# Kernel optimization log

Hardware: AMD Instinct MI355X
Metric: run time of the kernel (lower is better)

Reference implementation:

```python
import jax, jax.numpy as jnp
import numpy as np

B, C, H, W = 8, 16, 64, 64
O = 32
K = 3
STRIDE = 1
HO = (H - K) // STRIDE + 1  # 62
WO = (W - K) // STRIDE + 1  # 62
BIAS_VAL = 0.1


def setup_inputs() -> dict:
    key = jax.random.key(0)
    k1, k2 = jax.random.split(key)
    x = jax.random.normal(k1, (B, C, H, W), dtype=jnp.float32)
    # per-location weights: (1, O, C, Ho, Wo, K*K) in torch; drop leading 1
    weight = jax.random.normal(k2, (O, C, HO, WO, K * K), dtype=jnp.float32)
    bias = jnp.full((1, O, HO, WO), BIAS_VAL, dtype=jnp.float32)
    return {"x": x, "weight": weight, "bias": bias}


def _extract_patches(x):
    # emulate x.unfold(2,K,S).unfold(3,K,S).reshape(..., K*K)
    # patch index k = ki*K + kj
    patches = [
        x[:, :, ki:ki + (HO - 1) * STRIDE + 1:STRIDE, kj:kj + (WO - 1) * STRIDE + 1:STRIDE]
        for ki in range(K) for kj in range(K)
    ]
    return jnp.stack(patches, axis=-1)  # [B, C, Ho, Wo, K*K]


def reference(x, weight, bias):
    patches = _extract_patches(x)  # [B, C, Ho, Wo, K2]
    # (x.unsqueeze(1) * weight).sum([2, -1]) == contraction over C and K2 per location
    out = jnp.einsum('bchwk,ochwk->bohw', patches, weight)
    return out + bias
```

## Files before the change

kernel.cpp:

```cpp
#include <hip/hip_runtime.h>


#define BB 8
#define CC 16
#define HH 64
#define WW 64
#define OO 32
#define HO 62
#define WO 62
#define NLOC (HO * WO)
#define TOTAL (OO * NLOC)

__global__ __launch_bounds__(256) void lc2d_kernel(
    const float* __restrict__ x, const float* __restrict__ weight,
    const float* __restrict__ bias, float* __restrict__ out) {
  __shared__ float smem[4 * 576];

  const int tid  = threadIdx.x;
  const int lane = tid & 63;
  const int wave = tid >> 6;
  const int ho = blockIdx.x % HO;
  const int o  = blockIdx.x / HO;

  float* sw = smem + wave * 576;

  const int a1 = ((lane + 1) & 63) << 2;
  const int a2 = ((lane + 2) & 63) << 2;
  const int lidx = (lane < WO ? lane : WO - 1) * 9;

  float acc[BB];
#pragma unroll
  for (int b = 0; b < BB; ++b) acc[b] = 0.0f;

  for (int cc = 0; cc < 4; ++cc) {
    const int c = wave * 4 + cc;

    const float* wg = weight + (size_t)(o * CC + c) * (NLOC * 9) + (size_t)ho * (WO * 9);
#pragma unroll
    for (int j = 0; j < 9; ++j) {
      int idx = j * 64 + lane;
      if (idx < WO * 9) sw[idx] = wg[idx];
    }
    __syncthreads();

    float wreg[9];
#pragma unroll
    for (int k = 0; k < 9; ++k) wreg[k] = sw[lidx + k];

    const float* xc = x + (size_t)c * (HH * WW) + (size_t)ho * WW + lane;
#pragma unroll
    for (int b = 0; b < BB; ++b) {
      const float* xb = xc + (size_t)b * (CC * HH * WW);
      float v0 = xb[0];
      float v1 = xb[WW];
      float v2 = xb[2 * WW];
      float v0a = __int_as_float(__builtin_amdgcn_ds_bpermute(a1, __float_as_int(v0)));
      float v0b = __int_as_float(__builtin_amdgcn_ds_bpermute(a2, __float_as_int(v0)));
      float v1a = __int_as_float(__builtin_amdgcn_ds_bpermute(a1, __float_as_int(v1)));
      float v1b = __int_as_float(__builtin_amdgcn_ds_bpermute(a2, __float_as_int(v1)));
      float v2a = __int_as_float(__builtin_amdgcn_ds_bpermute(a1, __float_as_int(v2)));
      float v2b = __int_as_float(__builtin_amdgcn_ds_bpermute(a2, __float_as_int(v2)));
      acc[b] += v0 * wreg[0] + v0a * wreg[1] + v0b * wreg[2]
              + v1 * wreg[3] + v1a * wreg[4] + v1b * wreg[5]
              + v2 * wreg[6] + v2a * wreg[7] + v2b * wreg[8];
    }
    __syncthreads();
  }

#pragma unroll
  for (int b = 0; b < BB; ++b) sw[lane * 9 + b] = acc[b];
  __syncthreads();

  for (int p = tid; p < 512; p += 256) {
    int b = p >> 6;
    int l = p & 63;
    if (l < WO) {
      float s = smem[0 * 576 + l * 9 + b] + smem[1 * 576 + l * 9 + b]
              + smem[2 * 576 + l * 9 + b] + smem[3 * 576 + l * 9 + b];
      int loc = o * NLOC + ho * WO + l;
      out[(size_t)b * TOTAL + loc] = s + bias[loc];
    }
  }
}

extern "C" void kernel_launch(void* const* d_in, const int* in_sizes, int n_in,
                              void* d_out, int out_size, void* d_ws, size_t ws_size,
                              hipStream_t stream) {
  const float* x = (const float*)d_in[0];
  const float* w = (const float*)d_in[1];
  const float* bias = (const float*)d_in[2];
  float* out = (float*)d_out;

  hipLaunchKernelGGL(lc2d_kernel, dim3(OO * HO), dim3(256), 0, stream,
                     x, w, bias, out);
}
```

Baseline: 31.84 us.

## Double-buffer per-location weights with async global-to-LDS loads

Weight tiles for the next channel are now prefetched straight into a second LDS buffer with global_load_lds while the current channel is computed. This overlaps the weight stream with compute, removes the register round-trip, and drops one barrier per iteration. The batch loop is also split into two groups of four, so each group's x loads are issued together before the permutes and FMAs. The cost is double the LDS per block, and correctness depends on the async LDS writes having finished before the barrier.

```diff
diff --git a/kernel.cpp b/kernel.cpp
--- a/kernel.cpp
+++ b/kernel.cpp
@@ -11,10 +11,16 @@
 #define NLOC (HO * WO)
 #define TOTAL (OO * NLOC)
 
+__device__ __forceinline__ void async_f32_to_lds(const float* g, float* l) {
+  __builtin_amdgcn_global_load_lds((const __attribute__((address_space(1))) void*)g,
+                                   (__attribute__((address_space(3))) void*)l,
+                                   4, 0, 0);
+}
+
 __global__ __launch_bounds__(256) void lc2d_kernel(
     const float* __restrict__ x, const float* __restrict__ weight,
     const float* __restrict__ bias, float* __restrict__ out) {
-  __shared__ float smem[4 * 576];
+  __shared__ float smem[4 * 2 * 576];
 
   const int tid  = threadIdx.x;
   const int lane = tid & 63;
@@ -22,61 +28,100 @@
   const int ho = blockIdx.x % HO;
   const int o  = blockIdx.x / HO;
 
-  float* sw = smem + wave * 576;
+  float* buf0 = smem + wave * 1152;
+  float* buf1 = buf0 + 576;
 
   const int a1 = ((lane + 1) & 63) << 2;
   const int a2 = ((lane + 2) & 63) << 2;
   const int lidx = (lane < WO ? lane : WO - 1) * 9;
 
+  const float* wbase = weight + (size_t)(o * CC + wave * 4) * (NLOC * 9)
+                              + (size_t)ho * (WO * 9);
+
+#pragma unroll
+  for (int j = 0; j < 9; ++j) {
+    if (j * 64 + lane < WO * 9)
+      async_f32_to_lds(wbase + j * 64 + lane, buf0 + j * 64);
+  }
+
   float acc[BB];
 #pragma unroll
   for (int b = 0; b < BB; ++b) acc[b] = 0.0f;
 
+  const float* xw = x + (size_t)(wave * 4) * (HH * WW) + (size_t)ho * WW + lane;
+
+  __syncthreads();
+
+  float* cur = buf0;
+  float* nxt = buf1;
+
   for (int cc = 0; cc < 4; ++cc) {
-    const int c = wave * 4 + cc;
-
-    const float* wg = weight + (size_t)(o * CC + c) * (NLOC * 9) + (size_t)ho * (WO * 9);
+    if (cc < 3) {
+      const float* wg = wbase + (size_t)(cc + 1) * (NLOC * 9);
 #pragma unroll
-    for (int j = 0; j < 9; ++j) {
-      int idx = j * 64 + lane;
-      if (idx < WO * 9) sw[idx] = wg[idx];
+      for (int j = 0; j < 9; ++j) {
+        if (j * 64 + lane < WO * 9)
+          async_f32_to_lds(wg + j * 64 + lane, nxt + j * 64);
+      }
     }
-    __syncthreads();
 
     float wreg[9];
 #pragma unroll
-    for (int k = 0; k < 9; ++k) wreg[k] = sw[lidx + k];
+    for (int k = 0; k < 9; ++k) wreg[k] = cur[lidx + k];
 
-    const float* xc = x + (size_t)c * (HH * WW) + (size_t)ho * WW + lane;
+    const float* xc = xw + (size_t)cc * (HH * WW);
+
+    float v[4][3];
 #pragma unroll
-    for (int b = 0; b < BB; ++b) {
+    for (int b = 0; b < 4; ++b) {
       const float* xb = xc + (size_t)b * (CC * HH * WW);
-      float v0 = xb[0];
-      float v1 = xb[WW];
-      float v2 = xb[2 * WW];
-      float v0a = __int_as_float(__builtin_amdgcn_ds_bpermute(a1, __float_as_int(v0)));
-      float v0b = __int_as_float(__builtin_amdgcn_ds_bpermute(a2, __float_as_int(v0)));
-      float v1a = __int_as_float(__builtin_amdgcn_ds_bpermute(a1, __float_as_int(v1)));
-      float v1b = __int_as_float(__builtin_amdgcn_ds_bpermute(a2, __float_as_int(v1)));
-      float v2a = __int_as_float(__builtin_amdgcn_ds_bpermute(a1, __float_as_int(v2)));
-      float v2b = __int_as_float(__builtin_amdgcn_ds_bpermute(a2, __float_as_int(v2)));
-      acc[b] += v0 * wreg[0] + v0a * wreg[1] + v0b * wreg[2]
-              + v1 * wreg[3] + v1a * wreg[4] + v1b * wreg[5]
-              + v2 * wreg[6] + v2a * wreg[7] + v2b * wreg[8];
+      v[b][0] = xb[0]; v[b][1] = xb[WW]; v[b][2] = xb[2 * WW];
     }
+#pragma unroll
+    for (int b = 0; b < 4; ++b) {
+      float p01 = __int_as_float(__builtin_amdgcn_ds_bpermute(a1, __float_as_int(v[b][0])));
+      float p02 = __int_as_float(__builtin_amdgcn_ds_bpermute(a2, __float_as_int(v[b][0])));
+      float p11 = __int_as_float(__builtin_amdgcn_ds_bpermute(a1, __float_as_int(v[b][1])));
+      float p12 = __int_as_float(__builtin_amdgcn_ds_bpermute(a2, __float_as_int(v[b][1])));
+      float p21 = __int_as_float(__builtin_amdgcn_ds_bpermute(a1, __float_as_int(v[b][2])));
+      float p22 = __int_as_float(__builtin_amdgcn_ds_bpermute(a2, __float_as_int(v[b][2])));
+      acc[b] += v[b][0] * wreg[0] + p01 * wreg[1] + p02 * wreg[2]
+              + v[b][1] * wreg[3] + p11 * wreg[4] + p12 * wreg[5]
+              + v[b][2] * wreg[6] + p21 * wreg[7] + p22 * wreg[8];
+    }
+
+#pragma unroll
+    for (int b = 0; b < 4; ++b) {
+      const float* xb = xc + (size_t)(b + 4) * (CC * HH * WW);
+      v[b][0] = xb[0]; v[b][1] = xb[WW]; v[b][2] = xb[2 * WW];
+    }
+#pragma unroll
+    for (int b = 0; b < 4; ++b) {
+      float p01 = __int_as_float(__builtin_amdgcn_ds_bpermute(a1, __float_as_int(v[b][0])));
+      float p02 = __int_as_float(__builtin_amdgcn_ds_bpermute(a2, __float_as_int(v[b][0])));
+      float p11 = __int_as_float(__builtin_amdgcn_ds_bpermute(a1, __float_as_int(v[b][1])));
+      float p12 = __int_as_float(__builtin_amdgcn_ds_bpermute(a2, __float_as_int(v[b][1])));
+      float p21 = __int_as_float(__builtin_amdgcn_ds_bpermute(a1, __float_as_int(v[b][2])));
+      float p22 = __int_as_float(__builtin_amdgcn_ds_bpermute(a2, __float_as_int(v[b][2])));
+      acc[b + 4] += v[b][0] * wreg[0] + p01 * wreg[1] + p02 * wreg[2]
+                  + v[b][1] * wreg[3] + p11 * wreg[4] + p12 * wreg[5]
+                  + v[b][2] * wreg[6] + p21 * wreg[7] + p22 * wreg[8];
+    }
+
     __syncthreads();
+    float* t = cur; cur = nxt; nxt = t;
   }
 
 #pragma unroll
-  for (int b = 0; b < BB; ++b) sw[lane * 9 + b] = acc[b];
+  for (int b = 0; b < BB; ++b) buf0[lane * 9 + b] = acc[b];
   __syncthreads();
 
   for (int p = tid; p < 512; p += 256) {
     int b = p >> 6;
     int l = p & 63;
     if (l < WO) {
-      float s = smem[0 * 576 + l * 9 + b] + smem[1 * 576 + l * 9 + b]
-              + smem[2 * 576 + l * 9 + b] + smem[3 * 576 + l * 9 + b];
+      float s = smem[0 * 1152 + l * 9 + b] + smem[1 * 1152 + l * 9 + b]
+              + smem[2 * 1152 + l * 9 + b] + smem[3 * 1152 + l * 9 + b];
       int loc = o * NLOC + ho * WO + l;
       out[(size_t)b * TOTAL + loc] = s + bias[loc];
     }
```

New measurement: 30.81 us. -3.2%, faster.
